# Performance work log

Hardware: AMD Instinct MI355X
Metric: run time of the kernel (lower is better)

The kernel has to match this reference:

```python
import jax, jax.numpy as jnp
import numpy as np

H = 8
D_MODEL = 512
NEG = -1e9  # fp32 masking value from the torch source


def setup_inputs() -> dict:
    key = jax.random.key(0)
    ks = jax.random.split(key, 13)
    B, T, C, D = 2, 512, 8, D_MODEL
    s = 1.0 / np.sqrt(D)
    inp = {
        "query": jax.random.normal(ks[0], (B, T, C, D), jnp.float32),
        "key": jax.random.normal(ks[1], (B, T, C, D), jnp.float32),
        "value": jax.random.normal(ks[2], (B, T, C, D), jnp.float32),
        "mask": jax.random.randint(ks[3], (B, T, T, 1), 0, 2, jnp.int32),
        # four Linear(d_model, d_model) layers, stored as (in, out)
        "Wq": jax.random.normal(ks[4], (D, D), jnp.float32) * s,
        "bq": jax.random.normal(ks[5], (D,), jnp.float32) * s,
        "Wk": jax.random.normal(ks[6], (D, D), jnp.float32) * s,
        "bk": jax.random.normal(ks[7], (D,), jnp.float32) * s,
        "Wv": jax.random.normal(ks[8], (D, D), jnp.float32) * s,
        "bv": jax.random.normal(ks[9], (D,), jnp.float32) * s,
        "Wo": jax.random.normal(ks[10], (D, D), jnp.float32) * s,
        "bo": jax.random.normal(ks[11], (D,), jnp.float32) * s,
    }
    return inp


def _mha(query, key, value, mask, Wq, bq, Wk, bk, Wv, bv, Wo, bo):
    B, T, C, D = query.shape
    h, dk = H, D // H

    def proj(x, W, b):
        y = (x @ W + b).reshape(B, T, C, h, dk)
        return jnp.transpose(y, (0, 3, 2, 1, 4))  # [B,h,C,T,dk] (torch transpose(1,3))

    q = proj(query, Wq, bq)
    k = proj(key, Wk, bk)
    v = proj(value, Wv, bv)

    scores = jnp.einsum("bhctd,bhcsd->bhcts", q, k) / np.sqrt(dk)  # [B,h,C,T,T]
    # The torch view/transpose/view dance is just a permutation putting C last;
    # it is equivalent to masking scores[b,h,c,t,s] where mask[b,t,s,0]==0
    # (mask broadcast over heads h and channels c).
    m = mask[:, :, :, 0]  # [B,T,Tk]
    scores = jnp.where(m[:, None, None, :, :] == 0, NEG, scores)
    p_attn = jax.nn.softmax(scores, axis=-1)
    # dropout omitted (inference/deterministic reference)
    x = jnp.einsum("bhcts,bhcsd->bhctd", p_attn, v)  # [B,h,C,T,dk]
    x = jnp.transpose(x, (0, 3, 2, 1, 4)).reshape(B, T, C, D)
    return x @ Wo + bo


def reference(query, key, value, mask, Wq, bq, Wk, bk, Wv, bv, Wo, bo):
    return _mha(query, key, value, mask, Wq, bq, Wk, bk, Wv, bv, Wo, bo)
```

## Files before the change

kernel.cpp:

```cpp
#include <hip/hip_runtime.h>
#include <hip/hip_bf16.h>

typedef __bf16 bf16;
typedef __bf16 bf16x8 __attribute__((ext_vector_type(8)));
typedef float floatx4 __attribute__((ext_vector_type(4)));


#define AS1 __attribute__((address_space(1)))
#define AS3 __attribute__((address_space(3)))

__device__ __forceinline__ void gload_lds16(const bf16* g, bf16* l) {
    __builtin_amdgcn_global_load_lds((const AS1 unsigned int*)g,
                                     (AS3 unsigned int*)l, 16, 0, 0);
}

union Pack8 { bf16 h[8]; uint4 u; };
union Pack4 { bf16 h[4]; unsigned long long u; };

__device__ __forceinline__ void store_pack8(bf16* dst, float4 a, float4 b) {
    Pack8 p;
    p.h[0] = (bf16)a.x; p.h[1] = (bf16)a.y; p.h[2] = (bf16)a.z; p.h[3] = (bf16)a.w;
    p.h[4] = (bf16)b.x; p.h[5] = (bf16)b.y; p.h[6] = (bf16)b.z; p.h[7] = (bf16)b.w;
    *(uint4*)dst = p.u;
}

#define BAR_LG asm volatile("s_waitcnt lgkmcnt(0)\n\ts_barrier" ::: "memory")

__global__ __launch_bounds__(256) void wtr_kernel(
    const float* __restrict__ Wq, const float* __restrict__ Wk,
    const float* __restrict__ Wv, const float* __restrict__ Wo,
    bf16* __restrict__ WT)
{
    __shared__ float Ts[64][65];
    const int tid = threadIdx.x;
    const int k0 = blockIdx.x * 64;
    const int n0 = blockIdx.y * 64;
    const int z  = blockIdx.z;
    const float* W = (z == 0) ? Wq : (z == 1) ? Wk : (z == 2) ? Wv : Wo;
    bf16* O = WT + (size_t)z * 512 * 512;
    #pragma unroll
    for (int i = 0; i < 16; i++) {
        const int r = i * 4 + (tid >> 6), c = tid & 63;
        Ts[r][c] = W[(size_t)(k0 + r) * 512 + n0 + c];
    }
    __syncthreads();
    #pragma unroll
    for (int i = 0; i < 16; i++) {
        const int a = i * 4 + (tid >> 6), c = tid & 63;
        O[(size_t)(n0 + a) * 512 + k0 + c] = (bf16)Ts[c][a];
    }
}

__global__ __launch_bounds__(512, 3) void gemm_qkv(
    const float* __restrict__ Aq, const float* __restrict__ Ak,
    const float* __restrict__ Av, const bf16* __restrict__ WT,
    const float* __restrict__ Bq, const float* __restrict__ Bk,
    const float* __restrict__ Bv,
    bf16* __restrict__ Oq, bf16* __restrict__ Ok, bf16* __restrict__ Ov)
{
    __shared__ __align__(16) bf16 smem[17408];
    bf16* Asm = smem;
    bf16* Bsm = smem + 4096;

    const int z = blockIdx.z;
    const float* A    = (z == 0) ? Aq : (z == 1) ? Ak : Av;
    const float* bias = (z == 0) ? Bq : (z == 1) ? Bk : Bv;
    bf16* out         = (z == 0) ? Oq : (z == 1) ? Ok : Ov;
    const bf16* BT = WT + (size_t)z * 262144;
    const float scale = (z == 0) ? 0.125f : 1.0f;

    const int tid  = threadIdx.x;
    const int lane = tid & 63;
    const int wave = tid >> 6;
    const int quad = lane >> 4;
    const int l16  = lane & 15;
    const int mblk = blockIdx.x * 128;
    const int nblk = blockIdx.y * 256;

    const int srowA = tid >> 2;
    const int scolA = (tid & 3) * 8;
    const float* Ag = A + (size_t)(mblk + srowA) * 512 + scolA;
    const int aoff = srowA * 32 + scolA;
    const int srowB = wave * 16 + (lane >> 2);
    const int scolB = (lane & 3) * 8;
    const bf16* Bg0 = BT + (size_t)(nblk + srowB) * 512 + scolB;
    const bf16* Bg1 = Bg0 + (size_t)128 * 512;
    bf16* Bl0 = Bsm + wave * 16 * 32;
    bf16* Bl1 = Bsm + (128 + wave * 16) * 32;

    const int wr = (wave >> 2) * 64;
    const int wc = (wave & 3) * 64;

    floatx4 acc[4][4] = {};
    for (int k0 = 0; k0 < 512; k0 += 32) {
        gload_lds16(Bg0 + k0, Bl0);
        gload_lds16(Bg1 + k0, Bl1);
        float4 x0 = *(const float4*)(Ag + k0);
        float4 x1 = *(const float4*)(Ag + k0 + 4);
        store_pack8(Asm + aoff, x0, x1);
        __syncthreads();
        bf16x8 a[4], b[4];
        #pragma unroll
        for (int mt = 0; mt < 4; mt++)
            a[mt] = *(const bf16x8*)(Asm + (wr + mt * 16 + l16) * 32 + quad * 8);
        #pragma unroll
        for (int nt = 0; nt < 4; nt++)
            b[nt] = *(const bf16x8*)(Bsm + (wc + nt * 16 + l16) * 32 + quad * 8);
        #pragma unroll
        for (int mt = 0; mt < 4; mt++)
            #pragma unroll
            for (int nt = 0; nt < 4; nt++)
                acc[mt][nt] = __builtin_amdgcn_mfma_f32_16x16x32_bf16(
                    a[mt], b[nt], acc[mt][nt], 0, 0, 0);
        __syncthreads();
    }

    if (z != 2) {
        #pragma unroll
        for (int mt = 0; mt < 4; mt++) {
            #pragma unroll
            for (int nt = 0; nt < 4; nt++) {
                const int colg = nblk + wc + nt * 16 + l16;
                const float bb = bias[colg];
                #pragma unroll
                for (int r = 0; r < 4; r++) {
                    const int rowg = mblk + wr + mt * 16 + quad * 4 + r;
                    const float v = (acc[mt][nt][r] + bb) * scale;
                    const int b_ = rowg >> 12;
                    const int t_ = (rowg >> 3) & 511;
                    const int c  = rowg & 7;
                    const int h  = colg >> 6;
                    const int d  = colg & 63;
                    const int hd = b_ * 64 + h * 8 + c;
                    out[((size_t)hd * 512 + t_) * 64 + d] = (bf16)v;
                }
            }
        }
    } else {
        typedef bf16 TsmRow[136];
        TsmRow* Tsm = (TsmRow*)smem;
        const int b_ = mblk >> 12;
        const int t0 = (mblk >> 3) & 511;
        #pragma unroll
        for (int cb = 0; cb < 2; cb++) {
            if (((wave & 3) >> 1) == cb) {
                #pragma unroll
                for (int mt = 0; mt < 4; mt++) {
                    #pragma unroll
                    for (int nt = 0; nt < 4; nt++) {
                        const int clg = wc + nt * 16 + l16;
                        const float bb = bias[nblk + clg];
                        const int cl = clg - cb * 128;
                        #pragma unroll
                        for (int r = 0; r < 4; r++)
                            Tsm[wr + mt * 16 + quad * 4 + r][cl] =
                                (bf16)(acc[mt][nt][r] + bb);
                    }
                }
            }
            __syncthreads();
            #pragma unroll
            for (int e = tid; e < 1024; e += 512) {
                const int col = e >> 3, c = e & 7;
                const int gcol = nblk + cb * 128 + col;
                const int h = gcol >> 6, d = gcol & 63;
                const int hd = b_ * 64 + h * 8 + c;
                Pack8 lo, hi;
                #pragma unroll
                for (int j = 0; j < 8; j++) lo.h[j] = Tsm[j * 8 + c][col];
                #pragma unroll
                for (int j = 0; j < 8; j++) hi.h[j] = Tsm[(j + 8) * 8 + c][col];
                bf16* dst = out + ((size_t)hd * 64 + d) * 512 + t0;
                *(uint4*)dst = lo.u;
                *(uint4*)(dst + 8) = hi.u;
            }
            __syncthreads();
        }
    }
}

__global__ __launch_bounds__(512, 4) void gemm_o(
    const bf16* __restrict__ A, const bf16* __restrict__ BT,
    const float* __restrict__ bias, float* __restrict__ out)
{
    __shared__ __align__(16) bf16 smem[16384];
    bf16* Ab0 = smem;
    bf16* Ab1 = smem + 4096;
    bf16* Bb0 = smem + 8192;
    bf16* Bb1 = smem + 12288;

    const int tid  = threadIdx.x;
    const int lane = tid & 63;
    const int wave = tid >> 6;
    const int quad = lane >> 4;
    const int l16  = lane & 15;
    const int mblk = blockIdx.x * 128;
    const int nblk = blockIdx.y * 128;

    const int srow = wave * 16 + (lane >> 2);
    const int scol = (lane & 3) * 8;
    const bf16* Ag = A + (size_t)(mblk + srow) * 512 + scol;
    const bf16* Bg = BT + (size_t)(nblk + srow) * 512 + scol;
    const int aoff = srow * 32 + scol;

    const int wr = (wave >> 1) * 32;
    const int wc = (wave & 1) * 64;

    floatx4 acc[2][4] = {};

    uint4 xa = *(const uint4*)(Ag);
    uint4 xb = *(const uint4*)(Bg);
    *(uint4*)(Ab0 + aoff) = xa;
    *(uint4*)(Bb0 + aoff) = xb;
    uint4 ya = *(const uint4*)(Ag + 32);
    uint4 yb = *(const uint4*)(Bg + 32);
    *(uint4*)(Ab1 + aoff) = ya;
    *(uint4*)(Bb1 + aoff) = yb;
    xa = *(const uint4*)(Ag + 64);
    xb = *(const uint4*)(Bg + 64);
    BAR_LG;

    #pragma unroll
    for (int t = 0; t < 16; t++) {
        bf16* Ab = (t & 1) ? Ab1 : Ab0;
        bf16* Bb = (t & 1) ? Bb1 : Bb0;
        bf16x8 a[2], b[4];
        #pragma unroll
        for (int mt = 0; mt < 2; mt++)
            a[mt] = *(const bf16x8*)(Ab + (wr + mt * 16 + l16) * 32 + quad * 8);
        #pragma unroll
        for (int nt = 0; nt < 4; nt++)
            b[nt] = *(const bf16x8*)(Bb + (wc + nt * 16 + l16) * 32 + quad * 8);
        #pragma unroll
        for (int mt = 0; mt < 2; mt++)
            #pragma unroll
            for (int nt = 0; nt < 4; nt++)
                acc[mt][nt] = __builtin_amdgcn_mfma_f32_16x16x32_bf16(
                    a[mt], b[nt], acc[mt][nt], 0, 0, 0);
        if (t <= 12) {
            const int kL = (t + 3) * 32;
            if (t & 1) { xa = *(const uint4*)(Ag + kL); xb = *(const uint4*)(Bg + kL); }
            else       { ya = *(const uint4*)(Ag + kL); yb = *(const uint4*)(Bg + kL); }
        }
        BAR_LG;
        if (t <= 13) {
            if (t & 1) { *(uint4*)(Ab + aoff) = ya; *(uint4*)(Bb + aoff) = yb; }
            else       { *(uint4*)(Ab + aoff) = xa; *(uint4*)(Bb + aoff) = xb; }
        }
    }

    #pragma unroll
    for (int mt = 0; mt < 2; mt++) {
        #pragma unroll
        for (int nt = 0; nt < 4; nt++) {
            const int colg = nblk + wc + nt * 16 + l16;
            const float bb = bias[colg];
            #pragma unroll
            for (int r = 0; r < 4; r++) {
                const int rowg = mblk + wr + mt * 16 + quad * 4 + r;
                out[(size_t)rowg * 512 + colg] = acc[mt][nt][r] + bb;
            }
        }
    }
}

#define PST 520

__global__ __launch_bounds__(256, 2) void attn_kernel(
    const bf16* __restrict__ Qws, const bf16* __restrict__ Kws,
    const bf16* __restrict__ Vtws, const int* __restrict__ mask,
    bf16* __restrict__ Xws)
{
    __shared__ bf16 Psm[64][PST];
    __shared__ float redM[4][64];
    __shared__ float redS[4][64];
    const int tid  = threadIdx.x;
    const int wave = tid >> 6;
    const int lane = tid & 63;
    const int quad = lane >> 4;
    const int l16  = lane & 15;
    const int s_ = blockIdx.x;
    const int o_ = ((s_ & 7) << 7) | (s_ >> 3);
    const int hd = o_ >> 3;
    const int qt = o_ & 7;
    const int q0 = qt * 64;
    const int b = hd >> 6;
    const int h = (hd >> 3) & 7;
    const int c = hd & 7;

    const bf16* Qh = Qws + (size_t)hd * 512 * 64;
    const bf16* Kh = Kws + (size_t)hd * 512 * 64;
    const int* mp = mask + ((size_t)b * 512 + q0) * 512;

    bf16x8 aq[4][2];
    #pragma unroll
    for (int s = 0; s < 4; s++) {
        aq[s][0] = *(const bf16x8*)(Qh + (size_t)(q0 + s * 16 + l16) * 64 + quad * 8);
        aq[s][1] = *(const bf16x8*)(Qh + (size_t)(q0 + s * 16 + l16) * 64 + 32 + quad * 8);
    }

    floatx4 sv[4][8];
    #pragma unroll
    for (int s = 0; s < 4; s++)
        #pragma unroll
        for (int nt = 0; nt < 8; nt++)
            sv[s][nt] = (floatx4){0.f, 0.f, 0.f, 0.f};

    #pragma unroll
    for (int nt = 0; nt < 8; nt++) {
        const int s0 = wave * 128 + nt * 16;
        bf16x8 bk0 = *(const bf16x8*)(Kh + (size_t)(s0 + l16) * 64 + quad * 8);
        bf16x8 bk1 = *(const bf16x8*)(Kh + (size_t)(s0 + l16) * 64 + 32 + quad * 8);
        #pragma unroll
        for (int s = 0; s < 4; s++) {
            sv[s][nt] = __builtin_amdgcn_mfma_f32_16x16x32_bf16(
                bk0, aq[s][0], sv[s][nt], 0, 0, 0);
            sv[s][nt] = __builtin_amdgcn_mfma_f32_16x16x32_bf16(
                bk1, aq[s][1], sv[s][nt], 0, 0, 0);
        }
    }

    float mx[4] = {-3.0e38f, -3.0e38f, -3.0e38f, -3.0e38f};
    #pragma unroll
    for (int s = 0; s < 4; s++)
        #pragma unroll
        for (int nt = 0; nt < 8; nt++) {
            const int4 mv = *(const int4*)(
                mp + (size_t)(s * 16 + l16) * 512 + wave * 128 + nt * 16 + quad * 4);
            float v0 = sv[s][nt][0] + ((mv.x == 0) ? -1.0e9f : 0.0f);
            float v1 = sv[s][nt][1] + ((mv.y == 0) ? -1.0e9f : 0.0f);
            float v2 = sv[s][nt][2] + ((mv.z == 0) ? -1.0e9f : 0.0f);
            float v3 = sv[s][nt][3] + ((mv.w == 0) ? -1.0e9f : 0.0f);
            sv[s][nt][0] = v0; sv[s][nt][1] = v1;
            sv[s][nt][2] = v2; sv[s][nt][3] = v3;
            mx[s] = fmaxf(mx[s], fmaxf(fmaxf(v0, v1), fmaxf(v2, v3)));
        }
    #pragma unroll
    for (int s = 0; s < 4; s++) {
        mx[s] = fmaxf(mx[s], __shfl_xor(mx[s], 16, 64));
        mx[s] = fmaxf(mx[s], __shfl_xor(mx[s], 32, 64));
    }
    if (quad == 0)
        #pragma unroll
        for (int s = 0; s < 4; s++) redM[wave][s * 16 + l16] = mx[s];
    __syncthreads();

    float mf[4], sum[4] = {0.f, 0.f, 0.f, 0.f};
    #pragma unroll
    for (int s = 0; s < 4; s++) {
        const int qr = s * 16 + l16;
        mf[s] = fmaxf(fmaxf(redM[0][qr], redM[1][qr]),
                      fmaxf(redM[2][qr], redM[3][qr]));
    }
    #pragma unroll
    for (int s = 0; s < 4; s++)
        #pragma unroll
        for (int nt = 0; nt < 8; nt++)
            #pragma unroll
            for (int r = 0; r < 4; r++) {
                const float e = __expf(sv[s][nt][r] - mf[s]);
                sv[s][nt][r] = e;
                sum[s] += e;
            }
    #pragma unroll
    for (int s = 0; s < 4; s++) {
        sum[s] += __shfl_xor(sum[s], 16, 64);
        sum[s] += __shfl_xor(sum[s], 32, 64);
    }
    if (quad == 0)
        #pragma unroll
        for (int s = 0; s < 4; s++) redS[wave][s * 16 + l16] = sum[s];
    __syncthreads();

    float inv[4];
    #pragma unroll
    for (int s = 0; s < 4; s++) {
        const int qr = s * 16 + l16;
        inv[s] = 1.f / (redS[0][qr] + redS[1][qr] + redS[2][qr] + redS[3][qr]);
    }
    #pragma unroll
    for (int s = 0; s < 4; s++)
        #pragma unroll
        for (int nt = 0; nt < 8; nt++) {
            Pack4 pk;
            #pragma unroll
            for (int r = 0; r < 4; r++)
                pk.h[r] = (bf16)(sv[s][nt][r] * inv[s]);
            *(unsigned long long*)&Psm[s * 16 + l16][wave * 128 + nt * 16 + quad * 4]
                = pk.u;
        }
    __syncthreads();

    const bf16* Vh = Vtws + (size_t)hd * 64 * 512;
    const int d0 = wave * 16;
    floatx4 o[4] = {};
    #pragma unroll
    for (int ks = 0; ks < 16; ks++) {
        bf16x8 bv = *(const bf16x8*)(Vh + (size_t)(d0 + l16) * 512 + ks * 32 + quad * 8);
        #pragma unroll
        for (int rt = 0; rt < 4; rt++) {
            bf16x8 ap = *(const bf16x8*)(&Psm[rt * 16 + l16][ks * 32 + quad * 8]);
            o[rt] = __builtin_amdgcn_mfma_f32_16x16x32_bf16(ap, bv, o[rt], 0, 0, 0);
        }
    }
    #pragma unroll
    for (int rt = 0; rt < 4; rt++)
        #pragma unroll
        for (int r = 0; r < 4; r++) {
            const int q = q0 + rt * 16 + quad * 4 + r;
            const size_t row = ((size_t)b * 512 + q) * 8 + c;
            Xws[row * 512 + h * 64 + d0 + l16] = (bf16)o[rt][r];
        }
}

extern "C" void kernel_launch(void* const* d_in, const int* in_sizes, int n_in,
                              void* d_out, int out_size, void* d_ws, size_t ws_size,
                              hipStream_t stream)
{
    const float* qin  = (const float*)d_in[0];
    const float* kin  = (const float*)d_in[1];
    const float* vin  = (const float*)d_in[2];
    const int*   mask = (const int*)d_in[3];
    const float* Bq = (const float*)d_in[5];
    const float* Bk = (const float*)d_in[7];
    const float* Bv = (const float*)d_in[9];
    const float* Bo = (const float*)d_in[11];
    float* out = (float*)d_out;

    const size_t R = (size_t)8192 * 512;
    bf16* r0 = (bf16*)d_ws;
    bf16* r1 = r0 + R;
    bf16* r2 = r1 + R;
    bf16* r3 = r2 + R;
    bf16* WT = r3 + R;

    wtr_kernel<<<dim3(8, 8, 4), dim3(256), 0, stream>>>(
        (const float*)d_in[4], (const float*)d_in[6],
        (const float*)d_in[8], (const float*)d_in[10], WT);
    gemm_qkv<<<dim3(64, 2, 3), dim3(512), 0, stream>>>(
        qin, kin, vin, WT, Bq, Bk, Bv, r0, r1, r2);
    attn_kernel<<<dim3(1024), dim3(256), 0, stream>>>(
        r0, r1, r2, mask, r3);
    gemm_o<<<dim3(64, 4), dim3(512), 0, stream>>>(
        r3, WT + (size_t)3 * 262144, Bo, out);
}
```

Baseline: 190.4 us.

## Precompute bf16 additive mask and switch output GEMM to direct-to-LDS loads

Adds a small kernel that turns the int32 mask into a bf16 additive bias of -1e9 or 0. It writes this bias into the already-consumed Q/K slice of the weight workspace, and the attention kernel reads it with half the bytes and adds it without compare-select. The output projection GEMM now uses 64x128 tiles with 256 threads and global_load_lds into a single LDS buffer. That replaces the register-staged double-buffered pipeline and gives twice as many blocks. The cost is an extra launch, and the GEMM loses its overlap of loads with MFMA work because each k-step waits on its own loads.

```diff
diff --git a/kernel.cpp b/kernel.cpp
--- a/kernel.cpp
+++ b/kernel.cpp
@@ -23,8 +23,6 @@
     p.h[4] = (bf16)b.x; p.h[5] = (bf16)b.y; p.h[6] = (bf16)b.z; p.h[7] = (bf16)b.w;
     *(uint4*)dst = p.u;
 }
-
-#define BAR_LG asm volatile("s_waitcnt lgkmcnt(0)\n\ts_barrier" ::: "memory")
 
 __global__ __launch_bounds__(256) void wtr_kernel(
     const float* __restrict__ Wq, const float* __restrict__ Wk,
@@ -49,6 +47,24 @@
         const int a = i * 4 + (tid >> 6), c = tid & 63;
         O[(size_t)(n0 + a) * 512 + k0 + c] = (bf16)Ts[c][a];
     }
+}
+
+__global__ __launch_bounds__(256) void mask_cvt(
+    const int* __restrict__ m, bf16* __restrict__ o)
+{
+    const size_t i = ((size_t)blockIdx.x * 256 + threadIdx.x) * 8;
+    const int4 a = *(const int4*)(m + i);
+    const int4 b = *(const int4*)(m + i + 4);
+    Pack8 p;
+    p.h[0] = (a.x == 0) ? (bf16)(-1.0e9f) : (bf16)0.0f;
+    p.h[1] = (a.y == 0) ? (bf16)(-1.0e9f) : (bf16)0.0f;
+    p.h[2] = (a.z == 0) ? (bf16)(-1.0e9f) : (bf16)0.0f;
+    p.h[3] = (a.w == 0) ? (bf16)(-1.0e9f) : (bf16)0.0f;
+    p.h[4] = (b.x == 0) ? (bf16)(-1.0e9f) : (bf16)0.0f;
+    p.h[5] = (b.y == 0) ? (bf16)(-1.0e9f) : (bf16)0.0f;
+    p.h[6] = (b.z == 0) ? (bf16)(-1.0e9f) : (bf16)0.0f;
+    p.h[7] = (b.w == 0) ? (bf16)(-1.0e9f) : (bf16)0.0f;
+    *(uint4*)(o + i) = p.u;
 }
 
 __global__ __launch_bounds__(512, 3) void gemm_qkv(
@@ -179,74 +195,52 @@
     }
 }
 
-__global__ __launch_bounds__(512, 4) void gemm_o(
+__global__ __launch_bounds__(256) void gemm_o(
     const bf16* __restrict__ A, const bf16* __restrict__ BT,
     const float* __restrict__ bias, float* __restrict__ out)
 {
-    __shared__ __align__(16) bf16 smem[16384];
-    bf16* Ab0 = smem;
-    bf16* Ab1 = smem + 4096;
-    bf16* Bb0 = smem + 8192;
-    bf16* Bb1 = smem + 12288;
-
+    __shared__ bf16 Asm[64 * 32];
+    __shared__ bf16 Bsm[128 * 32];
     const int tid  = threadIdx.x;
     const int lane = tid & 63;
     const int wave = tid >> 6;
     const int quad = lane >> 4;
     const int l16  = lane & 15;
-    const int mblk = blockIdx.x * 128;
+    const int mblk = blockIdx.x * 64;
     const int nblk = blockIdx.y * 128;
 
     const int srow = wave * 16 + (lane >> 2);
     const int scol = (lane & 3) * 8;
-    const bf16* Ag = A + (size_t)(mblk + srow) * 512 + scol;
-    const bf16* Bg = BT + (size_t)(nblk + srow) * 512 + scol;
-    const int aoff = srow * 32 + scol;
+    const bf16* Ag  = A + (size_t)(mblk + srow) * 512 + scol;
+    const bf16* Bg0 = BT + (size_t)(nblk + srow) * 512 + scol;
+    const bf16* Bg1 = Bg0 + (size_t)64 * 512;
+    bf16* Al  = Asm + wave * 16 * 32;
+    bf16* Bl0 = Bsm + wave * 16 * 32;
+    bf16* Bl1 = Bsm + (64 + wave * 16) * 32;
 
     const int wr = (wave >> 1) * 32;
     const int wc = (wave & 1) * 64;
 
     floatx4 acc[2][4] = {};
-
-    uint4 xa = *(const uint4*)(Ag);
-    uint4 xb = *(const uint4*)(Bg);
-    *(uint4*)(Ab0 + aoff) = xa;
-    *(uint4*)(Bb0 + aoff) = xb;
-    uint4 ya = *(const uint4*)(Ag + 32);
-    uint4 yb = *(const uint4*)(Bg + 32);
-    *(uint4*)(Ab1 + aoff) = ya;
-    *(uint4*)(Bb1 + aoff) = yb;
-    xa = *(const uint4*)(Ag + 64);
-    xb = *(const uint4*)(Bg + 64);
-    BAR_LG;
-
-    #pragma unroll
-    for (int t = 0; t < 16; t++) {
-        bf16* Ab = (t & 1) ? Ab1 : Ab0;
-        bf16* Bb = (t & 1) ? Bb1 : Bb0;
+    for (int k0 = 0; k0 < 512; k0 += 32) {
+        gload_lds16(Ag + k0,  Al);
+        gload_lds16(Bg0 + k0, Bl0);
+        gload_lds16(Bg1 + k0, Bl1);
+        __syncthreads();
         bf16x8 a[2], b[4];
         #pragma unroll
         for (int mt = 0; mt < 2; mt++)
-            a[mt] = *(const bf16x8*)(Ab + (wr + mt * 16 + l16) * 32 + quad * 8);
+            a[mt] = *(const bf16x8*)(Asm + (wr + mt * 16 + l16) * 32 + quad * 8);
         #pragma unroll
         for (int nt = 0; nt < 4; nt++)
-            b[nt] = *(const bf16x8*)(Bb + (wc + nt * 16 + l16) * 32 + quad * 8);
+            b[nt] = *(const bf16x8*)(Bsm + (wc + nt * 16 + l16) * 32 + quad * 8);
         #pragma unroll
         for (int mt = 0; mt < 2; mt++)
             #pragma unroll
             for (int nt = 0; nt < 4; nt++)
                 acc[mt][nt] = __builtin_amdgcn_mfma_f32_16x16x32_bf16(
                     a[mt], b[nt], acc[mt][nt], 0, 0, 0);
-        if (t <= 12) {
-            const int kL = (t + 3) * 32;
-            if (t & 1) { xa = *(const uint4*)(Ag + kL); xb = *(const uint4*)(Bg + kL); }
-            else       { ya = *(const uint4*)(Ag + kL); yb = *(const uint4*)(Bg + kL); }
-        }
-        BAR_LG;
-        if (t <= 13) {
-            if (t & 1) { *(uint4*)(Ab + aoff) = ya; *(uint4*)(Bb + aoff) = yb; }
-            else       { *(uint4*)(Ab + aoff) = xa; *(uint4*)(Bb + aoff) = xb; }
-        }
+        __syncthreads();
     }
 
     #pragma unroll
@@ -268,7 +262,7 @@
 
 __global__ __launch_bounds__(256, 2) void attn_kernel(
     const bf16* __restrict__ Qws, const bf16* __restrict__ Kws,
-    const bf16* __restrict__ Vtws, const int* __restrict__ mask,
+    const bf16* __restrict__ Vtws, const bf16* __restrict__ maskbf,
     bf16* __restrict__ Xws)
 {
     __shared__ bf16 Psm[64][PST];
@@ -290,7 +284,7 @@
 
     const bf16* Qh = Qws + (size_t)hd * 512 * 64;
     const bf16* Kh = Kws + (size_t)hd * 512 * 64;
-    const int* mp = mask + ((size_t)b * 512 + q0) * 512;
+    const bf16* mp = maskbf + ((size_t)b * 512 + q0) * 512;
 
     bf16x8 aq[4][2];
     #pragma unroll
@@ -325,12 +319,13 @@
     for (int s = 0; s < 4; s++)
         #pragma unroll
         for (int nt = 0; nt < 8; nt++) {
-            const int4 mv = *(const int4*)(
+            Pack4 mv;
+            mv.u = *(const unsigned long long*)(
                 mp + (size_t)(s * 16 + l16) * 512 + wave * 128 + nt * 16 + quad * 4);
-            float v0 = sv[s][nt][0] + ((mv.x == 0) ? -1.0e9f : 0.0f);
-            float v1 = sv[s][nt][1] + ((mv.y == 0) ? -1.0e9f : 0.0f);
-            float v2 = sv[s][nt][2] + ((mv.z == 0) ? -1.0e9f : 0.0f);
-            float v3 = sv[s][nt][3] + ((mv.w == 0) ? -1.0e9f : 0.0f);
+            float v0 = sv[s][nt][0] + (float)mv.h[0];
+            float v1 = sv[s][nt][1] + (float)mv.h[1];
+            float v2 = sv[s][nt][2] + (float)mv.h[2];
+            float v3 = sv[s][nt][3] + (float)mv.h[3];
             sv[s][nt][0] = v0; sv[s][nt][1] = v1;
             sv[s][nt][2] = v2; sv[s][nt][3] = v3;
             mx[s] = fmaxf(mx[s], fmaxf(fmaxf(v0, v1), fmaxf(v2, v3)));
@@ -439,8 +434,9 @@
         (const float*)d_in[8], (const float*)d_in[10], WT);
     gemm_qkv<<<dim3(64, 2, 3), dim3(512), 0, stream>>>(
         qin, kin, vin, WT, Bq, Bk, Bv, r0, r1, r2);
+    mask_cvt<<<dim3(256), dim3(256), 0, stream>>>(mask, WT);
     attn_kernel<<<dim3(1024), dim3(256), 0, stream>>>(
-        r0, r1, r2, mask, r3);
-    gemm_o<<<dim3(64, 4), dim3(512), 0, stream>>>(
+        r0, r1, r2, WT, r3);
+    gemm_o<<<dim3(128, 4), dim3(256), 0, stream>>>(
         r3, WT + (size_t)3 * 262144, Bo, out);
 }
```

Result: no change. 192.4 us (+1.1%).
